# Optimization experiments

Hardware: AMD Instinct MI355X
Metric: run time of the kernel (lower is better)

The kernel has to match this reference:

```python
import jax, jax.numpy as jnp
import numpy as np

B, D, H, W = 1, 4, 48, 48
C, NH = 256, 8
HD = C // NH
KD, KH, KW = 3, 5, 5
KVOL = KD * KH * KW
SCALE = HD ** -0.5


def _nbhd(L, k):
    """Neighborhood start indices (clamped to stay in-bounds, natten semantics)
    and relative-position-bias indices for one axis."""
    i = jnp.arange(L)
    start = jnp.clip(i - k // 2, 0, L - k)            # [L]
    idx = start[:, None] + jnp.arange(k)[None, :]     # [L,k] absolute neighbor index
    rel = idx - i[:, None] + (k - 1)                  # [L,k] rpb index in [0, 2k-2]
    return idx, rel


def setup_inputs() -> dict:
    key = jax.random.key(0)
    ks = jax.random.split(key, 5)
    s = 0.02
    return {
        "x": jax.random.normal(ks[0], (B, D, H, W, C), jnp.float32),
        "w_qkv": jax.random.normal(ks[1], (C, 3 * C), jnp.float32) * s,
        "b_qkv": jnp.zeros((3 * C,), jnp.float32),
        "rpb": jax.random.normal(ks[2], (NH, 2 * KD - 1, 2 * KH - 1, 2 * KW - 1), jnp.float32) * s,
        "w_proj": jax.random.normal(ks[3], (C, C), jnp.float32) * s,
        "b_proj": jnp.zeros((C,), jnp.float32),
    }


def _nat3d(q, k, v, rpb):
    # q,k,v: [B,NH,D,H,W,HD]; q already scaled
    idxD, relD = _nbhd(D, KD)
    idxH, relH = _nbhd(H, KH)
    idxW, relW = _nbhd(W, KW)
    iD = idxD[:, None, None, :, None, None]
    iH = idxH[None, :, None, None, :, None]
    iW = idxW[None, None, :, None, None, :]
    gk = k[:, :, iD, iH, iW]   # [B,NH,D,H,W,KD,KH,KW,HD]
    gv = v[:, :, iD, iH, iW]
    bias = rpb[:, relD[:, None, None, :, None, None],
                  relH[None, :, None, None, :, None],
                  relW[None, None, :, None, None, :]]  # [NH,D,H,W,KD,KH,KW]
    scores = jnp.einsum("bndyxc,bndyxtuvc->bndyxtuv", q, gk) + bias[None]
    flat = scores.reshape(*scores.shape[:5], KVOL)
    attn = jax.nn.softmax(flat, axis=-1).reshape(scores.shape)
    return jnp.einsum("bndyxtuv,bndyxtuvc->bndyxc", attn, gv)


def reference(x, w_qkv, b_qkv, rpb, w_proj, b_proj):
    qkv = (x @ w_qkv + b_qkv).reshape(B, D, H, W, 3, NH, HD)
    qkv = jnp.transpose(qkv, (4, 0, 5, 1, 2, 3, 6))  # [3,B,NH,D,H,W,HD]
    q, k, v = qkv[0] * SCALE, qkv[1], qkv[2]
    out = _nat3d(q, k, v, rpb)                       # [B,NH,D,H,W,HD]
    out = jnp.transpose(out, (0, 2, 3, 4, 1, 5)).reshape(B, D, H, W, C)
    return out @ w_proj + b_proj
```

## Files before the change

kernel.cpp:

```cpp
#include <hip/hip_runtime.h>

#define QK_SCALE 0.17677669529663687f
#define TOKENS 9216

typedef __attribute__((ext_vector_type(8))) __bf16 bf16x8;
typedef __attribute__((ext_vector_type(8))) unsigned short us8;
typedef __attribute__((ext_vector_type(4))) float f32x4;

static __device__ __forceinline__ unsigned short f2bf(float x) {
    unsigned int u = __float_as_uint(x);
    return (unsigned short)((u + 0x7FFFu + ((u >> 16) & 1u)) >> 16);
}
static __device__ __forceinline__ float bf2f(unsigned short u) {
    return __uint_as_float(((unsigned int)u) << 16);
}
static __device__ __forceinline__ bf16x8 ld_bf8(const unsigned short* p) {
    us8 u = *reinterpret_cast<const us8*>(p);
    return __builtin_bit_cast(bf16x8, u);
}

__global__ __launch_bounds__(256) void conv_prep(
    const float* __restrict__ x, const float* __restrict__ wqkv, const float* __restrict__ wproj,
    const float* __restrict__ rpb,
    unsigned short* __restrict__ xb, unsigned short* __restrict__ wqT,
    unsigned short* __restrict__ wpT, unsigned short* __restrict__ biasT)
{
    int b = blockIdx.x, t = threadIdx.x;
    if (b < 2304) {
        int idx = (b * 256 + t) * 4;
        float4 v = *reinterpret_cast<const float4*>(x + idx);
        ushort4 o;
        o.x = f2bf(v.x); o.y = f2bf(v.y); o.z = f2bf(v.z); o.w = f2bf(v.w);
        *reinterpret_cast<ushort4*>(xb + idx) = o;
    } else if (b < 3072) {
        int e = (b - 2304) * 256 + t;
        int n = e >> 8, k = e & 255;
        wqT[n * 256 + k] = f2bf(wqkv[k * 768 + n]);
    } else if (b < 3328) {
        int e = (b - 3072) * 256 + t;
        int n = e >> 8, k = e & 255;
        wpT[n * 256 + k] = f2bf(wproj[k * 256 + n]);
    } else {
        const int bid = b - 3328;
        const int cls = bid >> 3, h = bid & 7;
        const int d  = cls / 9;
        const int r  = cls % 9;
        const int yc = r / 3, xc = r % 3;
        const int by = (yc == 0) ? 0 : ((yc == 1) ? 5 : 11);
        const int bx = (xc == 0) ? 0 : ((xc == 1) ? 5 : 11);
        const int y0 = by * 4, x0 = bx * 4;
        const int base_d = min(max(d - 1, 0), 1);
        const int base_h = min(max(y0 - 2, 0), 40);
        const int base_w = min(max(x0 - 2, 0), 40);
        const int relD = base_d - d + 2;
        unsigned short* dst = biasT + (size_t)bid * 3072;
        for (int idx = t; idx < 3072; idx += 256) {
            int tok = idx / 192;
            int rem = idx - tok * 192;
            int w = rem / 96; rem -= w * 96;
            int g = rem / 24;
            int j = rem - g * 24;
            int i = j >> 2, rg = j & 3;
            int cand = w * 96 + i * 16 + g * 4 + rg;
            int y = y0 + (tok >> 2), xx = x0 + (tok & 3);
            int sh = min(max(y - 2, 0), 43), sw = min(max(xx - 2, 0), 43);
            int ld = cand >> 6, lh = (cand >> 3) & 7, lw = cand & 7;
            int t0 = lh - (sh - base_h), t1 = lw - (sw - base_w);
            bool valid = ((unsigned)t0 < 5u) && ((unsigned)t1 < 5u);
            unsigned short v = 0xFF80;
            if (valid) {
                int bi = (relD + ld) * 81 + (lh - (y - base_h) + 4) * 9 + (lw - (xx - base_w) + 4);
                v = f2bf(rpb[h * 405 + bi]);
            }
            dst[idx] = v;
        }
    }
}

template<int MF, int NF, int MODE>
__global__ __launch_bounds__(256) void gemm_mfma(
    const unsigned short* __restrict__ A, const unsigned short* __restrict__ BT,
    const float* __restrict__ bias,
    unsigned short* __restrict__ oq, unsigned short* __restrict__ ok,
    unsigned short* __restrict__ ov, float* __restrict__ of)
{
    const int tid = threadIdx.x;
    const int wid = tid >> 6, lane = tid & 63;
    const int wm = wid >> 1, wn = wid & 1;
    const int n15 = lane & 15, g = lane >> 4;

    const int nwg = gridDim.x * gridDim.y;
    const int id  = blockIdx.y * gridDim.x + blockIdx.x;
    const int nid = (id & 7) * (nwg >> 3) + (id >> 3);
    const int bxs = nid % gridDim.x, bys = nid / gridDim.x;

    const int m0 = bys * (MF * 32) + wm * (MF * 16);
    const int n0 = bxs * (NF * 32) + wn * (NF * 16);

    f32x4 acc[MF][NF];
    #pragma unroll
    for (int i = 0; i < MF; i++)
        #pragma unroll
        for (int j = 0; j < NF; j++)
            acc[i][j] = f32x4{0.f, 0.f, 0.f, 0.f};

    #pragma unroll
    for (int ks = 0; ks < 8; ++ks) {
        bf16x8 a[MF], b[NF];
        #pragma unroll
        for (int mt = 0; mt < MF; ++mt)
            a[mt] = ld_bf8(A + (size_t)(m0 + mt * 16 + n15) * 256 + ks * 32 + g * 8);
        #pragma unroll
        for (int nt = 0; nt < NF; ++nt)
            b[nt] = ld_bf8(BT + (size_t)(n0 + nt * 16 + n15) * 256 + ks * 32 + g * 8);
        #pragma unroll
        for (int mt = 0; mt < MF; ++mt)
            #pragma unroll
            for (int nt = 0; nt < NF; ++nt)
                acc[mt][nt] = __builtin_amdgcn_mfma_f32_16x16x32_bf16(b[nt], a[mt], acc[mt][nt], 0, 0, 0);
    }

    #pragma unroll
    for (int mt = 0; mt < MF; ++mt) {
        #pragma unroll
        for (int nt = 0; nt < NF; ++nt) {
            int tok = m0 + mt * 16 + n15;
            int nb  = n0 + nt * 16 + g * 4;
            float4 bv4 = *reinterpret_cast<const float4*>(bias + nb);
            float v0 = acc[mt][nt][0] + bv4.x;
            float v1 = acc[mt][nt][1] + bv4.y;
            float v2 = acc[mt][nt][2] + bv4.z;
            float v3 = acc[mt][nt][3] + bv4.w;
            if (MODE == 0) {
                int part = nb >> 8, c = nb & 255, hh = c >> 5, ch = c & 31;
                unsigned short* dst = (part == 0) ? oq : ((part == 1) ? ok : ov);
                if (part == 0) { v0 *= QK_SCALE; v1 *= QK_SCALE; v2 *= QK_SCALE; v3 *= QK_SCALE; }
                ushort4 o;
                o.x = f2bf(v0); o.y = f2bf(v1); o.z = f2bf(v2); o.w = f2bf(v3);
                *reinterpret_cast<ushort4*>(dst + ((size_t)hh * TOKENS + tok) * 32 + ch) = o;
            } else {
                float4 o = make_float4(v0, v1, v2, v3);
                *reinterpret_cast<float4*>(of + (size_t)tok * 256 + nb) = o;
            }
        }
    }
}

__global__ __launch_bounds__(128) void nat_attn_mfma(
    const unsigned short* __restrict__ qws, const unsigned short* __restrict__ kws,
    const unsigned short* __restrict__ vws, const unsigned short* __restrict__ biasT,
    unsigned short* __restrict__ aout)
{
    __shared__ unsigned short VT[32 * 200];
    __shared__ unsigned short Pl[16 * 200];
    __shared__ float red[2][16];

    const int tid = threadIdx.x;
    const int w = tid >> 6, lane = tid & 63;
    const int n15 = lane & 15, g = lane >> 4;

    int b = blockIdx.x;
    const int h = b & 7; b >>= 3;
    const int bx = b % 12; b /= 12;
    const int by = b % 12;
    const int d  = b / 12;
    const int y0 = by * 4, x0 = bx * 4;
    const int base_d = min(max(d - 1, 0), 1);
    const int base_h = min(max(y0 - 2, 0), 40);
    const int base_w = min(max(x0 - 2, 0), 40);

    const int yc = (by == 0) ? 0 : ((by == 11) ? 2 : 1);
    const int xc = (bx == 0) ? 0 : ((bx == 11) ? 2 : 1);
    const unsigned short* bT = biasT + (size_t)(((d * 9 + yc * 3 + xc) * 8 + h)) * 3072;

    const size_t hoff = (size_t)h * TOKENS * 32;
    const unsigned short* kb = kws + hoff;
    const unsigned short* vb = vws + hoff;
    const unsigned short* qb = qws + hoff;

    for (int id = tid; id < 768; id += 128) {
        int cand = id % 192, chg = id / 192;
        int ld = cand >> 6, lh = (cand >> 3) & 7, lw = cand & 7;
        int gt = (base_d + ld) * 2304 + (base_h + lh) * 48 + (base_w + lw);
        us8 u = *reinterpret_cast<const us8*>(vb + (size_t)gt * 32 + chg * 8);
        #pragma unroll
        for (int e = 0; e < 8; e++) VT[(chg * 8 + e) * 200 + cand] = u[e];
    }

    us8 bl[3];
    {
        const unsigned short* bp = bT + (size_t)(((n15 * 2 + w) * 4 + g) * 24);
        bl[0] = *reinterpret_cast<const us8*>(bp);
        bl[1] = *reinterpret_cast<const us8*>(bp + 8);
        bl[2] = *reinterpret_cast<const us8*>(bp + 16);
    }

    const int gtq = d * 2304 + (y0 + (n15 >> 2)) * 48 + (x0 + (n15 & 3));
    bf16x8 qf = ld_bf8(qb + (size_t)gtq * 32 + g * 8);

    f32x4 sf[6];
    #pragma unroll
    for (int i = 0; i < 6; ++i) {
        int cand = (w * 6 + i) * 16 + n15;
        int ld = cand >> 6, lh = (cand >> 3) & 7, lw = cand & 7;
        int gtc = (base_d + ld) * 2304 + (base_h + lh) * 48 + (base_w + lw);
        bf16x8 kf = ld_bf8(kb + (size_t)gtc * 32 + g * 8);
        sf[i] = __builtin_amdgcn_mfma_f32_16x16x32_bf16(kf, qf, f32x4{0.f, 0.f, 0.f, 0.f}, 0, 0, 0);
    }

    float s24 = 0.f;
    uint2 pq[6];
    #pragma unroll
    for (int i = 0; i < 6; ++i) {
        int j = i * 4;
        float e0 = __expf(sf[i][0] + bf2f(bl[(j + 0) >> 3][(j + 0) & 7]));
        float e1 = __expf(sf[i][1] + bf2f(bl[(j + 1) >> 3][(j + 1) & 7]));
        float e2 = __expf(sf[i][2] + bf2f(bl[(j + 2) >> 3][(j + 2) & 7]));
        float e3 = __expf(sf[i][3] + bf2f(bl[(j + 3) >> 3][(j + 3) & 7]));
        s24 += (e0 + e1) + (e2 + e3);
        pq[i].x = (__float_as_uint(e1) & 0xFFFF0000u) | (__float_as_uint(e0) >> 16);
        pq[i].y = (__float_as_uint(e3) & 0xFFFF0000u) | (__float_as_uint(e2) >> 16);
    }
    s24 += __shfl_xor(s24, 16);
    s24 += __shfl_xor(s24, 32);
    if (g == 0) red[w][n15] = s24;

    #pragma unroll
    for (int i = 0; i < 6; ++i)
        *reinterpret_cast<uint2*>(&Pl[n15 * 200 + w * 96 + i * 16 + g * 4]) = pq[i];
    __syncthreads();

    f32x4 oacc = f32x4{0.f, 0.f, 0.f, 0.f};
    #pragma unroll
    for (int ks = 0; ks < 6; ++ks) {
        bf16x8 vf = ld_bf8(&VT[(w * 16 + n15) * 200 + ks * 32 + g * 8]);
        bf16x8 pa = ld_bf8(&Pl[n15 * 200 + ks * 32 + g * 8]);
        oacc = __builtin_amdgcn_mfma_f32_16x16x32_bf16(vf, pa, oacc, 0, 0, 0);
    }
    {
        float inv = 1.f / (red[0][n15] + red[1][n15]);
        int gtr = d * 2304 + (y0 + (n15 >> 2)) * 48 + (x0 + (n15 & 3));
        ushort4 o;
        o.x = f2bf(oacc[0] * inv);
        o.y = f2bf(oacc[1] * inv);
        o.z = f2bf(oacc[2] * inv);
        o.w = f2bf(oacc[3] * inv);
        *reinterpret_cast<ushort4*>(aout + (size_t)gtr * 256 + h * 32 + w * 16 + g * 4) = o;
    }
}

extern "C" void kernel_launch(void* const* d_in, const int* in_sizes, int n_in,
                              void* d_out, int out_size, void* d_ws, size_t ws_size,
                              hipStream_t stream) {
    const float* x      = (const float*)d_in[0];
    const float* w_qkv  = (const float*)d_in[1];
    const float* b_qkv  = (const float*)d_in[2];
    const float* rpb    = (const float*)d_in[3];
    const float* w_proj = (const float*)d_in[4];
    const float* b_proj = (const float*)d_in[5];
    float* out = (float*)d_out;

    unsigned short* ws = (unsigned short*)d_ws;
    unsigned short* xb    = ws;
    unsigned short* wqT   = ws + (size_t)2359296;
    unsigned short* wpT   = ws + (size_t)2555904;
    unsigned short* qws   = ws + (size_t)2621440;
    unsigned short* kws   = ws + (size_t)4980736;
    unsigned short* vws   = ws + (size_t)7340032;
    unsigned short* aws   = ws + (size_t)9699328;
    unsigned short* biasT = ws + (size_t)12058624;

    conv_prep<<<dim3(3616), 256, 0, stream>>>(x, w_qkv, w_proj, rpb, xb, wqT, wpT, biasT);

    gemm_mfma<4, 4, 0><<<dim3(6, 72), 256, 0, stream>>>(xb, wqT, b_qkv, qws, kws, vws, nullptr);

    nat_attn_mfma<<<dim3(4608), 128, 0, stream>>>(qws, kws, vws, biasT, aws);

    gemm_mfma<2, 2, 1><<<dim3(4, 144), 256, 0, stream>>>(aws, wpT, b_proj, nullptr, nullptr, nullptr, out);
}
```

Measured before the change: 64.83 us.

## Fuse x bf16 conversion into QKV GEMM and pair depth slices per attention block

The separate pass converting x to bf16 is removed, and the QKV GEMM now reads fp32 x directly and converts it in registers. This drops a full read and write of the activations through global memory. The attention kernel now handles two depth slices per 256-thread block (d=2*dp and 2*dp+1), which share the same V tile in LDS because D=4 gives base_d equal to dp for both. That halves V staging and the number of blocks, in exchange for more fp32 traffic per GEMM tile load and more LDS per block.

```diff
diff --git a/kernel.cpp b/kernel.cpp
--- a/kernel.cpp
+++ b/kernel.cpp
@@ -18,30 +18,32 @@
     us8 u = *reinterpret_cast<const us8*>(p);
     return __builtin_bit_cast(bf16x8, u);
 }
+static __device__ __forceinline__ bf16x8 cvt_f32x8(const float* p) {
+    float4 a = *reinterpret_cast<const float4*>(p);
+    float4 b = *reinterpret_cast<const float4*>(p + 4);
+    bf16x8 r;
+    r[0] = (__bf16)a.x; r[1] = (__bf16)a.y; r[2] = (__bf16)a.z; r[3] = (__bf16)a.w;
+    r[4] = (__bf16)b.x; r[5] = (__bf16)b.y; r[6] = (__bf16)b.z; r[7] = (__bf16)b.w;
+    return r;
+}
 
 __global__ __launch_bounds__(256) void conv_prep(
-    const float* __restrict__ x, const float* __restrict__ wqkv, const float* __restrict__ wproj,
+    const float* __restrict__ wqkv, const float* __restrict__ wproj,
     const float* __restrict__ rpb,
-    unsigned short* __restrict__ xb, unsigned short* __restrict__ wqT,
-    unsigned short* __restrict__ wpT, unsigned short* __restrict__ biasT)
+    unsigned short* __restrict__ wqT, unsigned short* __restrict__ wpT,
+    unsigned short* __restrict__ biasT)
 {
     int b = blockIdx.x, t = threadIdx.x;
-    if (b < 2304) {
-        int idx = (b * 256 + t) * 4;
-        float4 v = *reinterpret_cast<const float4*>(x + idx);
-        ushort4 o;
-        o.x = f2bf(v.x); o.y = f2bf(v.y); o.z = f2bf(v.z); o.w = f2bf(v.w);
-        *reinterpret_cast<ushort4*>(xb + idx) = o;
-    } else if (b < 3072) {
-        int e = (b - 2304) * 256 + t;
+    if (b < 768) {
+        int e = b * 256 + t;
         int n = e >> 8, k = e & 255;
         wqT[n * 256 + k] = f2bf(wqkv[k * 768 + n]);
-    } else if (b < 3328) {
-        int e = (b - 3072) * 256 + t;
+    } else if (b < 1024) {
+        int e = (b - 768) * 256 + t;
         int n = e >> 8, k = e & 255;
         wpT[n * 256 + k] = f2bf(wproj[k * 256 + n]);
     } else {
-        const int bid = b - 3328;
+        const int bid = b - 1024;
         const int cls = bid >> 3, h = bid & 7;
         const int d  = cls / 9;
         const int r  = cls % 9;
@@ -57,11 +59,11 @@
         for (int idx = t; idx < 3072; idx += 256) {
             int tok = idx / 192;
             int rem = idx - tok * 192;
-            int w = rem / 96; rem -= w * 96;
+            int half = rem / 96; rem -= half * 96;
             int g = rem / 24;
             int j = rem - g * 24;
             int i = j >> 2, rg = j & 3;
-            int cand = w * 96 + i * 16 + g * 4 + rg;
+            int cand = half * 96 + i * 16 + g * 4 + rg;
             int y = y0 + (tok >> 2), xx = x0 + (tok & 3);
             int sh = min(max(y - 2, 0), 43), sw = min(max(xx - 2, 0), 43);
             int ld = cand >> 6, lh = (cand >> 3) & 7, lw = cand & 7;
@@ -79,8 +81,8 @@
 
 template<int MF, int NF, int MODE>
 __global__ __launch_bounds__(256) void gemm_mfma(
-    const unsigned short* __restrict__ A, const unsigned short* __restrict__ BT,
-    const float* __restrict__ bias,
+    const float* __restrict__ Af, const unsigned short* __restrict__ Ab,
+    const unsigned short* __restrict__ BT, const float* __restrict__ bias,
     unsigned short* __restrict__ oq, unsigned short* __restrict__ ok,
     unsigned short* __restrict__ ov, float* __restrict__ of)
 {
@@ -108,8 +110,12 @@
     for (int ks = 0; ks < 8; ++ks) {
         bf16x8 a[MF], b[NF];
         #pragma unroll
-        for (int mt = 0; mt < MF; ++mt)
-            a[mt] = ld_bf8(A + (size_t)(m0 + mt * 16 + n15) * 256 + ks * 32 + g * 8);
+        for (int mt = 0; mt < MF; ++mt) {
+            if (MODE == 0)
+                a[mt] = cvt_f32x8(Af + (size_t)(m0 + mt * 16 + n15) * 256 + ks * 32 + g * 8);
+            else
+                a[mt] = ld_bf8(Ab + (size_t)(m0 + mt * 16 + n15) * 256 + ks * 32 + g * 8);
+        }
         #pragma unroll
         for (int nt = 0; nt < NF; ++nt)
             b[nt] = ld_bf8(BT + (size_t)(n0 + nt * 16 + n15) * 256 + ks * 32 + g * 8);
@@ -146,26 +152,27 @@
     }
 }
 
-__global__ __launch_bounds__(128) void nat_attn_mfma(
+__global__ __launch_bounds__(256) void nat_attn_mfma(
     const unsigned short* __restrict__ qws, const unsigned short* __restrict__ kws,
     const unsigned short* __restrict__ vws, const unsigned short* __restrict__ biasT,
     unsigned short* __restrict__ aout)
 {
     __shared__ unsigned short VT[32 * 200];
-    __shared__ unsigned short Pl[16 * 200];
-    __shared__ float red[2][16];
+    __shared__ unsigned short Pl[2][16 * 200];
+    __shared__ float red[2][2][16];
 
     const int tid = threadIdx.x;
     const int w = tid >> 6, lane = tid & 63;
     const int n15 = lane & 15, g = lane >> 4;
+    const int pl = w >> 1, half = w & 1;
 
     int b = blockIdx.x;
     const int h = b & 7; b >>= 3;
     const int bx = b % 12; b /= 12;
     const int by = b % 12;
-    const int d  = b / 12;
+    const int dp = b / 12;
+    const int d  = dp * 2 + pl;
     const int y0 = by * 4, x0 = bx * 4;
-    const int base_d = min(max(d - 1, 0), 1);
     const int base_h = min(max(y0 - 2, 0), 40);
     const int base_w = min(max(x0 - 2, 0), 40);
 
@@ -178,10 +185,10 @@
     const unsigned short* vb = vws + hoff;
     const unsigned short* qb = qws + hoff;
 
-    for (int id = tid; id < 768; id += 128) {
+    for (int id = tid; id < 768; id += 256) {
         int cand = id % 192, chg = id / 192;
         int ld = cand >> 6, lh = (cand >> 3) & 7, lw = cand & 7;
-        int gt = (base_d + ld) * 2304 + (base_h + lh) * 48 + (base_w + lw);
+        int gt = (dp + ld) * 2304 + (base_h + lh) * 48 + (base_w + lw);
         us8 u = *reinterpret_cast<const us8*>(vb + (size_t)gt * 32 + chg * 8);
         #pragma unroll
         for (int e = 0; e < 8; e++) VT[(chg * 8 + e) * 200 + cand] = u[e];
@@ -189,7 +196,7 @@
 
     us8 bl[3];
     {
-        const unsigned short* bp = bT + (size_t)(((n15 * 2 + w) * 4 + g) * 24);
+        const unsigned short* bp = bT + (size_t)(((n15 * 2 + half) * 4 + g) * 24);
         bl[0] = *reinterpret_cast<const us8*>(bp);
         bl[1] = *reinterpret_cast<const us8*>(bp + 8);
         bl[2] = *reinterpret_cast<const us8*>(bp + 16);
@@ -201,9 +208,9 @@
     f32x4 sf[6];
     #pragma unroll
     for (int i = 0; i < 6; ++i) {
-        int cand = (w * 6 + i) * 16 + n15;
+        int cand = (half * 6 + i) * 16 + n15;
         int ld = cand >> 6, lh = (cand >> 3) & 7, lw = cand & 7;
-        int gtc = (base_d + ld) * 2304 + (base_h + lh) * 48 + (base_w + lw);
+        int gtc = (dp + ld) * 2304 + (base_h + lh) * 48 + (base_w + lw);
         bf16x8 kf = ld_bf8(kb + (size_t)gtc * 32 + g * 8);
         sf[i] = __builtin_amdgcn_mfma_f32_16x16x32_bf16(kf, qf, f32x4{0.f, 0.f, 0.f, 0.f}, 0, 0, 0);
     }
@@ -223,29 +230,29 @@
     }
     s24 += __shfl_xor(s24, 16);
     s24 += __shfl_xor(s24, 32);
-    if (g == 0) red[w][n15] = s24;
+    if (g == 0) red[pl][half][n15] = s24;
 
     #pragma unroll
     for (int i = 0; i < 6; ++i)
-        *reinterpret_cast<uint2*>(&Pl[n15 * 200 + w * 96 + i * 16 + g * 4]) = pq[i];
+        *reinterpret_cast<uint2*>(&Pl[pl][n15 * 200 + half * 96 + i * 16 + g * 4]) = pq[i];
     __syncthreads();
 
     f32x4 oacc = f32x4{0.f, 0.f, 0.f, 0.f};
     #pragma unroll
     for (int ks = 0; ks < 6; ++ks) {
-        bf16x8 vf = ld_bf8(&VT[(w * 16 + n15) * 200 + ks * 32 + g * 8]);
-        bf16x8 pa = ld_bf8(&Pl[n15 * 200 + ks * 32 + g * 8]);
+        bf16x8 vf = ld_bf8(&VT[(half * 16 + n15) * 200 + ks * 32 + g * 8]);
+        bf16x8 pa = ld_bf8(&Pl[pl][n15 * 200 + ks * 32 + g * 8]);
         oacc = __builtin_amdgcn_mfma_f32_16x16x32_bf16(vf, pa, oacc, 0, 0, 0);
     }
     {
-        float inv = 1.f / (red[0][n15] + red[1][n15]);
+        float inv = 1.f / (red[pl][0][n15] + red[pl][1][n15]);
         int gtr = d * 2304 + (y0 + (n15 >> 2)) * 48 + (x0 + (n15 & 3));
         ushort4 o;
         o.x = f2bf(oacc[0] * inv);
         o.y = f2bf(oacc[1] * inv);
         o.z = f2bf(oacc[2] * inv);
         o.w = f2bf(oacc[3] * inv);
-        *reinterpret_cast<ushort4*>(aout + (size_t)gtr * 256 + h * 32 + w * 16 + g * 4) = o;
+        *reinterpret_cast<ushort4*>(aout + (size_t)gtr * 256 + h * 32 + half * 16 + g * 4) = o;
     }
 }
 
@@ -261,20 +268,19 @@
     float* out = (float*)d_out;
 
     unsigned short* ws = (unsigned short*)d_ws;
-    unsigned short* xb    = ws;
-    unsigned short* wqT   = ws + (size_t)2359296;
-    unsigned short* wpT   = ws + (size_t)2555904;
-    unsigned short* qws   = ws + (size_t)2621440;
-    unsigned short* kws   = ws + (size_t)4980736;
-    unsigned short* vws   = ws + (size_t)7340032;
-    unsigned short* aws   = ws + (size_t)9699328;
-    unsigned short* biasT = ws + (size_t)12058624;
-
-    conv_prep<<<dim3(3616), 256, 0, stream>>>(x, w_qkv, w_proj, rpb, xb, wqT, wpT, biasT);
-
-    gemm_mfma<4, 4, 0><<<dim3(6, 72), 256, 0, stream>>>(xb, wqT, b_qkv, qws, kws, vws, nullptr);
-
-    nat_attn_mfma<<<dim3(4608), 128, 0, stream>>>(qws, kws, vws, biasT, aws);
-
-    gemm_mfma<2, 2, 1><<<dim3(4, 144), 256, 0, stream>>>(aws, wpT, b_proj, nullptr, nullptr, nullptr, out);
-}
+    unsigned short* wqT   = ws;
+    unsigned short* wpT   = ws + (size_t)196608;
+    unsigned short* qws   = ws + (size_t)262144;
+    unsigned short* kws   = ws + (size_t)2621440;
+    unsigned short* vws   = ws + (size_t)4980736;
+    unsigned short* aws   = ws + (size_t)7340032;
+    unsigned short* biasT = ws + (size_t)9699328;
+
+    conv_prep<<<dim3(1312), 256, 0, stream>>>(w_qkv, w_proj, rpb, wqT, wpT, biasT);
+
+    gemm_mfma<4, 4, 0><<<dim3(6, 72), 256, 0, stream>>>(x, nullptr, wqT, b_qkv, qws, kws, vws, nullptr);
+
+    nat_attn_mfma<<<dim3(2304), 256, 0, stream>>>(qws, kws, vws, biasT, aws);
+
+    gemm_mfma<2, 2, 1><<<dim3(4, 144), 256, 0, stream>>>(nullptr, aws, wpT, b_proj, nullptr, nullptr, nullptr, out);
+}
```

After: 65.64 us. No clear change (+1.2%).
